# Performance work log

Hardware: AMD Instinct MI355X
Metric: run time of the kernel (lower is better)

Reference implementation:

```python
import jax, jax.numpy as jnp
import numpy as np


def setup_inputs() -> dict:
    key = jax.random.key(0)
    kq, kk, kv = jax.random.split(key, 3)
    B, S, D = 8, 4096, 64
    q = jax.random.normal(kq, (B, S, D), dtype=jnp.float32)
    k = jax.random.normal(kk, (B, S, D), dtype=jnp.float32)
    v = jax.random.normal(kv, (B, S, D), dtype=jnp.float32)
    mask = jnp.ones((B, S), dtype=jnp.float32)
    return {"q": q, "k": k, "v": v, "mask": mask}


def reference(q, k, v, mask):
    # scores: [B, Sq, Sk], scaled by sqrt(D)
    scale = 1.0 / jnp.sqrt(jnp.asarray(q.shape[-1], q.dtype))
    w = jnp.einsum("bqd,bkd->bqk", q, k) * scale
    # softmax over dim=2 (keys axis for rank-3 input)
    w = jax.nn.softmax(w, axis=2)
    x = jnp.einsum("bqk,bkd->bqd", w, v)
    # post-hoc multiplicative mask on outputs
    x = x * mask[..., None]
    return x
```

## Files before the change

kernel.cpp:

```cpp
#include <hip/hip_runtime.h>

typedef __attribute__((ext_vector_type(8))) short short8;
typedef __attribute__((ext_vector_type(4))) short short4v;
typedef __attribute__((ext_vector_type(4))) float floatx4;
typedef __attribute__((ext_vector_type(4))) unsigned short ushortx4;
typedef __attribute__((ext_vector_type(8))) unsigned short ushortx8;
typedef unsigned int u32;
typedef __attribute__((ext_vector_type(2))) u32 u32x2;
typedef __attribute__((ext_vector_type(4))) u32 u32x4;

#define MFMA_K32(A, B, C) __builtin_amdgcn_mfma_f32_16x16x32_bf16(A, B, C, 0, 0, 0)

#if __has_builtin(__builtin_amdgcn_mfma_f32_16x16x16bf16_1k)
#define HAVE_K16 1
#define MFMA_K16(A, B, C) __builtin_amdgcn_mfma_f32_16x16x16bf16_1k(A, B, C, 0, 0, 0)
#else
#define HAVE_K16 0
#endif

#if __has_builtin(__builtin_amdgcn_exp2f)
#define EXP2(x) __builtin_amdgcn_exp2f(x)
#else
#define EXP2(x) exp2f(x)
#endif

#define WAIT_VM6() __builtin_amdgcn_s_waitcnt(0x0F76)
#define WAIT_VM0() __builtin_amdgcn_s_waitcnt(0x0F70)
#define SB0() __builtin_amdgcn_sched_barrier(0)

__device__ __forceinline__ unsigned short f2bf(float f) {
  u32 u = __builtin_bit_cast(u32, f);
  u += 0x7FFFu + ((u >> 16) & 1u);
  return (unsigned short)(u >> 16);
}
__device__ __forceinline__ void load_lds16(const void* g, void* l) {
  __builtin_amdgcn_global_load_lds((const __attribute__((address_space(1))) u32*)g,
                                   (__attribute__((address_space(3))) u32*)l, 16, 0, 0);
}

__global__ __launch_bounds__(256) void prep_kv(
    const float* __restrict__ k, const float* __restrict__ v,
    unsigned short* __restrict__ kb, unsigned short* __restrict__ vt) {
  __shared__ float tileT[64 * 68];
  const int blk = blockIdx.x, tid = threadIdx.x;
  size_t base = (size_t)blk * 4096 + tid * 4;
#pragma unroll
  for (int i = 0; i < 4; i++) {
    size_t off = base + (size_t)i * 1024;
    floatx4 f = *(const floatx4*)(k + off);
    ushortx4 h;
    h[0] = f2bf(f[0]); h[1] = f2bf(f[1]); h[2] = f2bf(f[2]); h[3] = f2bf(f[3]);
    *(ushortx4*)(kb + off) = h;
  }
  const int r = tid >> 2, c4 = (tid & 3) * 16;
  const float* vp = v + ((size_t)blk * 64 + r) * 64 + c4;
#pragma unroll
  for (int i = 0; i < 4; i++) {
    floatx4 f = *(const floatx4*)(vp + i * 4);
#pragma unroll
    for (int j = 0; j < 4; j++) tileT[(c4 + i * 4 + j) * 68 + r] = f[j];
  }
  __syncthreads();
  unsigned short* vo = vt + (size_t)blk * 4096;
#pragma unroll
  for (int i = 0; i < 2; i++) {
    const int u = tid + i * 256;
    const int w = u >> 7, d = (u >> 1) & 63, half = u & 1;
    const float* src = tileT + d * 68 + w * 16 + half * 8;
    floatx4 f0 = *(const floatx4*)src;
    floatx4 f1 = *(const floatx4*)(src + 4);
    ushortx8 h;
#pragma unroll
    for (int j = 0; j < 4; j++) { h[j] = f2bf(f0[j]); h[4 + j] = f2bf(f1[j]); }
    *(ushortx8*)(vo + u * 8) = h;
  }
}

__global__ __launch_bounds__(256, 2) void attn(
    const float* __restrict__ q, const unsigned short* __restrict__ kb,
    const unsigned short* __restrict__ vt, const float* __restrict__ mask,
    float* __restrict__ out) {
  __shared__ __align__(16) char smem_raw[37888];
  unsigned short* smem = (unsigned short*)smem_raw;
  const int tid = threadIdx.x;
  const int wave = tid >> 6, lane = tid & 63;
  const int c = lane & 15, quad = lane >> 4;
  const int b = blockIdx.x & 7, qt = blockIdx.x >> 3;
  const int q0 = qt * 64;

  const unsigned short* kB = kb + (size_t)b * (4096 * 64);
  const unsigned short* vtB = vt + (size_t)b * (64 * 4096);

  const float qscale = 0.18033688011112042f;
  short8 qf[4][2];
#pragma unroll
  for (int nt = 0; nt < 4; nt++)
#pragma unroll
    for (int kc = 0; kc < 2; kc++) {
      const float* qp = q + ((size_t)b * 4096 + q0 + nt * 16 + c) * 64 + kc * 32 + quad * 8;
      floatx4 f0 = *(const floatx4*)qp;
      floatx4 f1 = *(const floatx4*)(qp + 4);
      short8 s;
#pragma unroll
      for (int j = 0; j < 4; j++) {
        s[j] = (short)f2bf(f0[j] * qscale);
        s[4 + j] = (short)f2bf(f1[j] * qscale);
      }
      qf[nt][kc] = s;
    }

  floatx4 o[4][4], o_l[4];
#pragma unroll
  for (int mt = 0; mt < 4; mt++)
#pragma unroll
    for (int nt = 0; nt < 4; nt++) o[mt][nt] = (floatx4){0.f, 0.f, 0.f, 0.f};
#pragma unroll
  for (int nt = 0; nt < 4; nt++) o_l[nt] = (floatx4){0.f, 0.f, 0.f, 0.f};

#if HAVE_K16
  short4v ones_a;
#pragma unroll
  for (int j = 0; j < 4; j++) ones_a[j] = (short)0x3F80;
#else
  short8 ones_a;
#pragma unroll
  for (int j = 0; j < 8; j++) ones_a[j] = (short)0x3F80;
#endif

  const int r8 = lane >> 3, cs8 = lane & 7;
  unsigned short* wbase = smem + wave * 2048;
  const unsigned short* gK0 = kB + (size_t)(wave * 16 + r8) * 64 + (cs8 ^ r8) * 8;
  const unsigned short* gV0 = vtB + wave * 1024;
  const int voff = (c * 16 + quad * 4);

  auto stageK = [&](int t, int buf) {
    unsigned short* Kd = wbase + buf * 1024;
    const unsigned short* gk = gK0 + (size_t)t * 4096;
    load_lds16(gk, Kd);
    load_lds16(gk + 8 * 64, Kd + 512);
  };
  auto loadV = [&](u32x2* vv, int t) {
    const unsigned short* gv = gV0 + (size_t)t * 4096 + voff;
#pragma unroll
    for (int mt = 0; mt < 4; mt++) vv[mt] = *(const u32x2*)(gv + mt * 256);
  };

  auto compute = [&](const unsigned short* Kbuf, const u32x2* vv) {
    short8 kf[2];
#pragma unroll
    for (int kc = 0; kc < 2; kc++)
      kf[kc] = *(const short8*)(Kbuf + c * 64 + ((kc * 4 + quad) ^ (c & 7)) * 8);
#pragma unroll
    for (int nt = 0; nt < 4; nt++) {
      floatx4 s = (floatx4){0.f, 0.f, 0.f, 0.f};
      s = MFMA_K32(kf[0], qf[nt][0], s);
      s = MFMA_K32(kf[1], qf[nt][1], s);
      u32 u0 = __builtin_bit_cast(u32, EXP2(s[0]));
      u32 u1 = __builtin_bit_cast(u32, EXP2(s[1]));
      u32 u2 = __builtin_bit_cast(u32, EXP2(s[2]));
      u32 u3 = __builtin_bit_cast(u32, EXP2(s[3]));
      u32 plo = __builtin_amdgcn_perm(u1, u0, 0x07060302u);
      u32 phi = __builtin_amdgcn_perm(u3, u2, 0x07060302u);
#if HAVE_K16
      short4v pf = __builtin_bit_cast(short4v, (u32x2){plo, phi});
#pragma unroll
      for (int mt = 0; mt < 4; mt++)
        o[mt][nt] = MFMA_K16(__builtin_bit_cast(short4v, vv[mt]), pf, o[mt][nt]);
      o_l[nt] = MFMA_K16(ones_a, pf, o_l[nt]);
#else
      short8 pf = __builtin_bit_cast(short8, (u32x4){plo, phi, 0u, 0u});
#pragma unroll
      for (int mt = 0; mt < 4; mt++) {
        short8 va = __builtin_bit_cast(short8, (u32x4){vv[mt][0], vv[mt][1], 0u, 0u});
        o[mt][nt] = MFMA_K32(va, pf, o[mt][nt]);
      }
      o_l[nt] = MFMA_K32(ones_a, pf, o_l[nt]);
#endif
    }
  };

  u32x2 vvA[4], vvB[4];
  stageK(0, 0);
  loadV(vvA, 0);

#pragma unroll 1
  for (int tt = 0; tt < 32; tt++) {
    const int t0 = 2 * tt, t1 = t0 + 1;
    stageK(t1, 1);
    loadV(vvB, t1);
    WAIT_VM6();
    SB0();
    compute(wbase, vvA);
    if (tt < 31) {
      stageK(t0 + 2, 0);
      loadV(vvA, t0 + 2);
      WAIT_VM6();
    } else {
      WAIT_VM0();
    }
    SB0();
    compute(wbase + 1024, vvB);
  }

  __syncthreads();
  float* obuf = (float*)smem_raw;
  float* lbuf = obuf + 9216;
  if (lane < 16) {
#pragma unroll
    for (int nt = 0; nt < 4; nt++) lbuf[wave * 64 + nt * 16 + c] = o_l[nt][0];
  }
  if (wave < 2) {
    float* ob = obuf + wave * 4608;
#pragma unroll
    for (int mt = 0; mt < 4; mt++)
#pragma unroll
      for (int nt = 0; nt < 4; nt++)
        *(floatx4*)(ob + (nt * 16 + c) * 72 + mt * 16 + quad * 4) = o[mt][nt];
  }
  __syncthreads();
  if (wave >= 2) {
    float* ob = obuf + (wave - 2) * 4608;
#pragma unroll
    for (int mt = 0; mt < 4; mt++)
#pragma unroll
      for (int nt = 0; nt < 4; nt++) {
        float* a = ob + (nt * 16 + c) * 72 + mt * 16 + quad * 4;
        floatx4 cur = *(floatx4*)a;
        *(floatx4*)a = cur + o[mt][nt];
      }
  }
  __syncthreads();

  const int row = tid >> 2, dg = (tid & 3) * 16;
  const float l = lbuf[row] + lbuf[64 + row] + lbuf[128 + row] + lbuf[192 + row];
  const float sc = mask[b * 4096 + q0 + row] / l;
  float* op = out + ((size_t)b * 4096 + q0 + row) * 64 + dg;
#pragma unroll
  for (int i = 0; i < 4; i++) {
    floatx4 a = *(const floatx4*)(obuf + row * 72 + dg + i * 4);
    floatx4 b2 = *(const floatx4*)(obuf + 4608 + row * 72 + dg + i * 4);
    *(floatx4*)(op + i * 4) = (a + b2) * sc;
  }
}

extern "C" void kernel_launch(void* const* d_in, const int* in_sizes, int n_in,
                              void* d_out, int out_size, void* d_ws, size_t ws_size,
                              hipStream_t stream) {
  const float* q = (const float*)d_in[0];
  const float* k = (const float*)d_in[1];
  const float* v = (const float*)d_in[2];
  const float* mask = (const float*)d_in[3];
  unsigned short* kb = (unsigned short*)d_ws;
  unsigned short* vt = kb + 8 * 4096 * 64;
  prep_kv<<<512, 256, 0, stream>>>(k, v, kb, vt);
  attn<<<512, 256, 0, stream>>>(q, kb, vt, mask, (float*)d_out);
}
```

Before: 125.4 us.

## Double per-wave key tile to 32 and use full K32 MFMA for PV

Each wave now processes 32 keys per step instead of 16, so the P·V product uses the 16x16x32 bf16 MFMA with a full 8-element P fragment rather than the K16 variant. The V transpose layout in the prep kernel is reorganized to match 32-key chunks, and K staging moves to a 4-deep LDS ring with an extra prefetch stage and adjusted waitcnt thresholds. This halves loop iterations and MFMA issue count for PV, and deepens the prefetch to hide load latency. In exchange LDS per block grows to 64KB, which may limit occupancy, and register pressure rises from the wider V fragments.

```diff
diff --git a/kernel.cpp b/kernel.cpp
--- a/kernel.cpp
+++ b/kernel.cpp
@@ -1,7 +1,6 @@
 #include <hip/hip_runtime.h>
 
 typedef __attribute__((ext_vector_type(8))) short short8;
-typedef __attribute__((ext_vector_type(4))) short short4v;
 typedef __attribute__((ext_vector_type(4))) float floatx4;
 typedef __attribute__((ext_vector_type(4))) unsigned short ushortx4;
 typedef __attribute__((ext_vector_type(8))) unsigned short ushortx8;
@@ -11,20 +10,14 @@
 
 #define MFMA_K32(A, B, C) __builtin_amdgcn_mfma_f32_16x16x32_bf16(A, B, C, 0, 0, 0)
 
-#if __has_builtin(__builtin_amdgcn_mfma_f32_16x16x16bf16_1k)
-#define HAVE_K16 1
-#define MFMA_K16(A, B, C) __builtin_amdgcn_mfma_f32_16x16x16bf16_1k(A, B, C, 0, 0, 0)
-#else
-#define HAVE_K16 0
-#endif
-
 #if __has_builtin(__builtin_amdgcn_exp2f)
 #define EXP2(x) __builtin_amdgcn_exp2f(x)
 #else
 #define EXP2(x) exp2f(x)
 #endif
 
-#define WAIT_VM6() __builtin_amdgcn_s_waitcnt(0x0F76)
+#define WAIT_VM12() __builtin_amdgcn_s_waitcnt(0x0F7C)
+#define WAIT_VM8() __builtin_amdgcn_s_waitcnt(0x0F78)
 #define WAIT_VM0() __builtin_amdgcn_s_waitcnt(0x0F70)
 #define SB0() __builtin_amdgcn_sched_barrier(0)
 
@@ -52,8 +45,9 @@
     h[0] = f2bf(f[0]); h[1] = f2bf(f[1]); h[2] = f2bf(f[2]); h[3] = f2bf(f[3]);
     *(ushortx4*)(kb + off) = h;
   }
+  const int b = blk >> 6, h = blk & 63;
   const int r = tid >> 2, c4 = (tid & 3) * 16;
-  const float* vp = v + ((size_t)blk * 64 + r) * 64 + c4;
+  const float* vp = v + ((size_t)b * 4096 + h * 64 + r) * 64 + c4;
 #pragma unroll
   for (int i = 0; i < 4; i++) {
     floatx4 f = *(const floatx4*)(vp + i * 4);
@@ -61,18 +55,17 @@
     for (int j = 0; j < 4; j++) tileT[(c4 + i * 4 + j) * 68 + r] = f[j];
   }
   __syncthreads();
-  unsigned short* vo = vt + (size_t)blk * 4096;
-#pragma unroll
-  for (int i = 0; i < 2; i++) {
-    const int u = tid + i * 256;
-    const int w = u >> 7, d = (u >> 1) & 63, half = u & 1;
-    const float* src = tileT + d * 68 + w * 16 + half * 8;
+  const int d = tid >> 2, g = tid & 3;
+  unsigned short* vb = vt + (size_t)b * 262144 + ((h >> 1) * 4 + (h & 1) * 2) * 2048;
+#pragma unroll
+  for (int s = 0; s < 2; s++) {
+    const float* src = tileT + d * 68 + s * 32 + g * 8;
     floatx4 f0 = *(const floatx4*)src;
     floatx4 f1 = *(const floatx4*)(src + 4);
-    ushortx8 h;
-#pragma unroll
-    for (int j = 0; j < 4; j++) { h[j] = f2bf(f0[j]); h[4 + j] = f2bf(f1[j]); }
-    *(ushortx8*)(vo + u * 8) = h;
+    ushortx8 hh;
+#pragma unroll
+    for (int j = 0; j < 4; j++) { hh[j] = f2bf(f0[j]); hh[4 + j] = f2bf(f1[j]); }
+    *(ushortx8*)(vb + s * 2048 + d * 32 + g * 8) = hh;
   }
 }
 
@@ -80,7 +73,7 @@
     const float* __restrict__ q, const unsigned short* __restrict__ kb,
     const unsigned short* __restrict__ vt, const float* __restrict__ mask,
     float* __restrict__ out) {
-  __shared__ __align__(16) char smem_raw[37888];
+  __shared__ __align__(16) char smem_raw[65536];
   unsigned short* smem = (unsigned short*)smem_raw;
   const int tid = threadIdx.x;
   const int wave = tid >> 6, lane = tid & 63;
@@ -89,7 +82,7 @@
   const int q0 = qt * 64;
 
   const unsigned short* kB = kb + (size_t)b * (4096 * 64);
-  const unsigned short* vtB = vt + (size_t)b * (64 * 4096);
+  const unsigned short* vtB = vt + (size_t)b * 262144;
 
   const float qscale = 0.18033688011112042f;
   short8 qf[4][2];
@@ -117,89 +110,82 @@
 #pragma unroll
   for (int nt = 0; nt < 4; nt++) o_l[nt] = (floatx4){0.f, 0.f, 0.f, 0.f};
 
-#if HAVE_K16
-  short4v ones_a;
-#pragma unroll
-  for (int j = 0; j < 4; j++) ones_a[j] = (short)0x3F80;
-#else
-  short8 ones_a;
-#pragma unroll
-  for (int j = 0; j < 8; j++) ones_a[j] = (short)0x3F80;
-#endif
+  short8 ones8;
+#pragma unroll
+  for (int j = 0; j < 8; j++) ones8[j] = (short)0x3F80;
 
   const int r8 = lane >> 3, cs8 = lane & 7;
-  unsigned short* wbase = smem + wave * 2048;
-  const unsigned short* gK0 = kB + (size_t)(wave * 16 + r8) * 64 + (cs8 ^ r8) * 8;
-  const unsigned short* gV0 = vtB + wave * 1024;
-  const int voff = (c * 16 + quad * 4);
+  const int klane = (r8 >> 2) * 8 + (r8 & 3);
+  unsigned short* wbase = smem + wave * 8192;
+  const unsigned short* gK0 = kB + (size_t)(wave * 32 + klane) * 64 + (cs8 ^ r8) * 8;
+  const unsigned short* gV0 = vtB + wave * 2048 + c * 32 + quad * 8;
 
   auto stageK = [&](int t, int buf) {
-    unsigned short* Kd = wbase + buf * 1024;
-    const unsigned short* gk = gK0 + (size_t)t * 4096;
+    unsigned short* Kd = wbase + buf * 2048;
+    const unsigned short* gk = gK0 + (size_t)t * 8192;
     load_lds16(gk, Kd);
-    load_lds16(gk + 8 * 64, Kd + 512);
+    load_lds16(gk + 16 * 64, Kd + 512);
+    load_lds16(gk + 4 * 64, Kd + 1024);
+    load_lds16(gk + 20 * 64, Kd + 1536);
   };
-  auto loadV = [&](u32x2* vv, int t) {
-    const unsigned short* gv = gV0 + (size_t)t * 4096 + voff;
-#pragma unroll
-    for (int mt = 0; mt < 4; mt++) vv[mt] = *(const u32x2*)(gv + mt * 256);
+  auto loadV = [&](u32x4* vv, int t) {
+    const unsigned short* gv = gV0 + (size_t)t * 8192;
+#pragma unroll
+    for (int mt = 0; mt < 4; mt++) vv[mt] = *(const u32x4*)(gv + mt * 512);
   };
 
-  auto compute = [&](const unsigned short* Kbuf, const u32x2* vv) {
-    short8 kf[2];
-#pragma unroll
-    for (int kc = 0; kc < 2; kc++)
-      kf[kc] = *(const short8*)(Kbuf + c * 64 + ((kc * 4 + quad) ^ (c & 7)) * 8);
+  auto compute = [&](const unsigned short* Kbuf, const u32x4* vv) {
+    short8 kfA[2], kfB[2];
+#pragma unroll
+    for (int kc = 0; kc < 2; kc++) {
+      const int sl = ((kc * 4 + quad) ^ (c & 7)) * 8;
+      kfA[kc] = *(const short8*)(Kbuf + c * 64 + sl);
+      kfB[kc] = *(const short8*)(Kbuf + 1024 + c * 64 + sl);
+    }
 #pragma unroll
     for (int nt = 0; nt < 4; nt++) {
-      floatx4 s = (floatx4){0.f, 0.f, 0.f, 0.f};
-      s = MFMA_K32(kf[0], qf[nt][0], s);
-      s = MFMA_K32(kf[1], qf[nt][1], s);
-      u32 u0 = __builtin_bit_cast(u32, EXP2(s[0]));
-      u32 u1 = __builtin_bit_cast(u32, EXP2(s[1]));
-      u32 u2 = __builtin_bit_cast(u32, EXP2(s[2]));
-      u32 u3 = __builtin_bit_cast(u32, EXP2(s[3]));
-      u32 plo = __builtin_amdgcn_perm(u1, u0, 0x07060302u);
-      u32 phi = __builtin_amdgcn_perm(u3, u2, 0x07060302u);
-#if HAVE_K16
-      short4v pf = __builtin_bit_cast(short4v, (u32x2){plo, phi});
+      floatx4 sA = (floatx4){0.f, 0.f, 0.f, 0.f}, sB = sA;
+      sA = MFMA_K32(kfA[0], qf[nt][0], sA);
+      sA = MFMA_K32(kfA[1], qf[nt][1], sA);
+      sB = MFMA_K32(kfB[0], qf[nt][0], sB);
+      sB = MFMA_K32(kfB[1], qf[nt][1], sB);
+      u32 a0 = __builtin_bit_cast(u32, EXP2(sA[0]));
+      u32 a1 = __builtin_bit_cast(u32, EXP2(sA[1]));
+      u32 a2 = __builtin_bit_cast(u32, EXP2(sA[2]));
+      u32 a3 = __builtin_bit_cast(u32, EXP2(sA[3]));
+      u32 b0 = __builtin_bit_cast(u32, EXP2(sB[0]));
+      u32 b1 = __builtin_bit_cast(u32, EXP2(sB[1]));
+      u32 b2 = __builtin_bit_cast(u32, EXP2(sB[2]));
+      u32 b3 = __builtin_bit_cast(u32, EXP2(sB[3]));
+      u32x4 pw = {__builtin_amdgcn_perm(a1, a0, 0x07060302u),
+                  __builtin_amdgcn_perm(a3, a2, 0x07060302u),
+                  __builtin_amdgcn_perm(b1, b0, 0x07060302u),
+                  __builtin_amdgcn_perm(b3, b2, 0x07060302u)};
+      short8 pf = __builtin_bit_cast(short8, pw);
 #pragma unroll
       for (int mt = 0; mt < 4; mt++)
-        o[mt][nt] = MFMA_K16(__builtin_bit_cast(short4v, vv[mt]), pf, o[mt][nt]);
-      o_l[nt] = MFMA_K16(ones_a, pf, o_l[nt]);
-#else
-      short8 pf = __builtin_bit_cast(short8, (u32x4){plo, phi, 0u, 0u});
-#pragma unroll
-      for (int mt = 0; mt < 4; mt++) {
-        short8 va = __builtin_bit_cast(short8, (u32x4){vv[mt][0], vv[mt][1], 0u, 0u});
-        o[mt][nt] = MFMA_K32(va, pf, o[mt][nt]);
-      }
-      o_l[nt] = MFMA_K32(ones_a, pf, o_l[nt]);
-#endif
+        o[mt][nt] = MFMA_K32(__builtin_bit_cast(short8, vv[mt]), pf, o[mt][nt]);
+      o_l[nt] = MFMA_K32(ones8, pf, o_l[nt]);
     }
   };
 
-  u32x2 vvA[4], vvB[4];
+  u32x4 vvA[4], vvB[4];
   stageK(0, 0);
   loadV(vvA, 0);
+  stageK(1, 1);
 
 #pragma unroll 1
-  for (int tt = 0; tt < 32; tt++) {
+  for (int tt = 0; tt < 16; tt++) {
     const int t0 = 2 * tt, t1 = t0 + 1;
-    stageK(t1, 1);
     loadV(vvB, t1);
-    WAIT_VM6();
+    if (t0 + 2 < 32) { stageK(t0 + 2, (t0 + 2) & 3); WAIT_VM12(); }
+    else { WAIT_VM8(); }
     SB0();
-    compute(wbase, vvA);
-    if (tt < 31) {
-      stageK(t0 + 2, 0);
-      loadV(vvA, t0 + 2);
-      WAIT_VM6();
-    } else {
-      WAIT_VM0();
-    }
+    compute(wbase + (t0 & 3) * 2048, vvA);
+    if (t1 + 2 < 32) { loadV(vvA, t1 + 1); stageK(t1 + 2, (t1 + 2) & 3); WAIT_VM12(); }
+    else { WAIT_VM0(); }
     SB0();
-    compute(wbase + 1024, vvB);
+    compute(wbase + (t1 & 3) * 2048, vvB);
   }
 
   __syncthreads();
```

Measured after the change: 115.9 us. 1.08x faster.
